# Optimization experiments

Measured on AMD Instinct MI355X. Metric: run time of the kernel, lower is better.

## Reference

```python
import jax, jax.numpy as jnp
import numpy as np

N_NODES = 100000


def _l2norm(v, eps=1e-12):
    return v / (jnp.linalg.norm(v) + eps)


def setup_inputs() -> dict:
    key = jax.random.key(0)
    k1, k2, k3, k4 = jax.random.split(key, 4)
    x = jax.random.normal(k1, (N_NODES, 128), dtype=jnp.float32)
    edge_index = jax.random.randint(k2, (2, 600000), 0, N_NODES, dtype=jnp.int64)
    # GCNConv weight [in, out] (xavier-ish scale), bias zeros (default init)
    W = jax.random.normal(k3, (128, 64), dtype=jnp.float32) * (1.0 / np.sqrt(128))
    bias = jnp.zeros((64,), dtype=jnp.float32)
    # learnable edge_wt initialized to ones (torch.ones_like(edge_weight))
    ew = jnp.ones((600000,), dtype=jnp.float32)
    # spectral-norm persistent power-iteration vector u (len = W.shape[0])
    u = jax.random.normal(k4, (128,), dtype=jnp.float32)
    return {"x": x, "edge_index": edge_index, "W": W, "bias": bias, "ew": ew, "u": u}


def gcn_forward(x, edge_index, W, bias, ew, u):
    N = x.shape[0]
    # --- spectral norm: one power-iteration step (u, v under stop_gradient) ---
    v = jax.lax.stop_gradient(_l2norm(W.T @ u))          # [out]
    u2 = jax.lax.stop_gradient(_l2norm(W @ v))           # [in]
    sigma = u2 @ (W @ v)
    W_sn = W / sigma
    # --- GCNConv with sigmoid edge weights, self-loops (weight 1), sym norm ---
    w = jax.nn.sigmoid(ew)                               # [E]
    row, col = edge_index[0], edge_index[1]
    deg = jax.ops.segment_sum(w, col, num_segments=N) + 1.0  # +1 from self-loop
    dis = jax.lax.rsqrt(deg)                             # deg > 0 always
    xp = x @ W_sn                                        # [N, out]
    norm_e = dis[row] * w * dis[col]                     # [E]
    msg = xp[row] * norm_e[:, None]                      # gather + scale
    agg = jax.ops.segment_sum(msg, col, num_segments=N)  # scatter-add
    out = agg + xp * (1.0 / deg)[:, None] + bias         # self-loop norm = deg^-1
    return out


def reference(x, edge_index, W, bias, ew, u):
    return gcn_forward(x, edge_index, W, bias, ew, u)
```

## Files before the change

kernel.cpp:

```cpp
#include <hip/hip_runtime.h>
#include <math.h>


#define IN_DIM 128
#define OUT_DIM 64

#define FIXSHIFT 4294967296.0
#define CNTSHIFT 40
#define DEGMASK  ((1ull << CNTSHIFT) - 1)

typedef __attribute__((ext_vector_type(4))) short s16x4;
typedef __attribute__((ext_vector_type(8))) short s16x8;
typedef __attribute__((ext_vector_type(4))) float f32x4;

__device__ __forceinline__ short f2bf(float f) {
    unsigned int v = __float_as_uint(f);
    v = v + 0x7FFFu + ((v >> 16) & 1u);
    return (short)(v >> 16);
}
__device__ __forceinline__ float bfLo(unsigned int v) {
    return __uint_as_float(v << 16);
}
__device__ __forceinline__ float bfHi(unsigned int v) {
    return __uint_as_float(v & 0xFFFF0000u);
}

#define APITCH 136

__global__ __launch_bounds__(256) void edge_prep(const int* __restrict__ ei,
                                                 const float* __restrict__ ew,
                                                 unsigned long long* __restrict__ packed,
                                                 int* __restrict__ slot,
                                                 int E) {
    const int e = blockIdx.x * 256 + threadIdx.x;
    if (e >= E) return;
    const float w = 1.f / (1.f + expf(-ew[e]));
    const int col = ei[E + e];
    const unsigned long long inc =
        (1ull << CNTSHIFT) | (unsigned long long)((double)w * FIXSHIFT);
    const unsigned long long old = atomicAdd(&packed[col], inc);
    slot[e] = (int)(old >> CNTSHIFT);
}

__global__ __launch_bounds__(256) void gemm_fused(const float* __restrict__ x,
                                                  const float* __restrict__ W,
                                                  const float* __restrict__ u,
                                                  const unsigned long long* __restrict__ packed,
                                                  unsigned short* __restrict__ xps,
                                                  int* __restrict__ pos,
                                                  int* __restrict__ btot,
                                                  float* __restrict__ inv_sigma,
                                                  int N, int NB) {
    __shared__ __align__(16) short As[64 * APITCH];
    __shared__ __align__(16) short Wt[64 * APITCH];

    const int t = threadIdx.x;
    const int bid = blockIdx.x;
    const int ntile = (N + 63) >> 6;

    if (bid < ntile) {
        const int r0 = bid * 64;
        {
            const int rl = t >> 2;
            const int qk = t & 3;
            const int grow = min(r0 + rl, N - 1);
            const float4* src = (const float4*)(x + (size_t)grow * IN_DIM + qk * 32);
            short* dst = &As[rl * APITCH + qk * 32];
            #pragma unroll
            for (int i = 0; i < 8; ++i) {
                const float4 v = src[i];
                s16x4 s4;
                s4.x = f2bf(v.x); s4.y = f2bf(v.y);
                s4.z = f2bf(v.z); s4.w = f2bf(v.w);
                *(s16x4*)(dst + i * 4) = s4;
            }
        }
        {
            #pragma unroll
            for (int p = 0; p < 2; ++p) {
                const int k  = p * 64 + (t >> 2);
                const int n0 = (t & 3) * 16;
                const float4* wsrc = (const float4*)(W + (size_t)k * OUT_DIM + n0);
                #pragma unroll
                for (int i = 0; i < 4; ++i) {
                    const float4 v = wsrc[i];
                    Wt[(n0 + 4 * i + 0) * APITCH + k] = f2bf(v.x);
                    Wt[(n0 + 4 * i + 1) * APITCH + k] = f2bf(v.y);
                    Wt[(n0 + 4 * i + 2) * APITCH + k] = f2bf(v.z);
                    Wt[(n0 + 4 * i + 3) * APITCH + k] = f2bf(v.w);
                }
            }
        }
        __syncthreads();

        const int wave = t >> 6;
        const int lane = t & 63;
        const int m    = lane & 15;
        const int quad = lane >> 4;

        f32x4 acc[4];
        #pragma unroll
        for (int ct = 0; ct < 4; ++ct) acc[ct] = (f32x4){0.f, 0.f, 0.f, 0.f};

        const short* Abase = &As[(wave * 16 + m) * APITCH + quad * 8];
        const short* Bbase = &Wt[m * APITCH + quad * 8];

        #pragma unroll
        for (int kc = 0; kc < 4; ++kc) {
            const s16x8 a = *(const s16x8*)(Abase + kc * 32);
            #pragma unroll
            for (int ct = 0; ct < 4; ++ct) {
                const s16x8 b = *(const s16x8*)(Bbase + ct * 16 * APITCH + kc * 32);
                acc[ct] = __builtin_amdgcn_mfma_f32_16x16x32_bf16(a, b, acc[ct], 0, 0, 0);
            }
        }

        #pragma unroll
        for (int r = 0; r < 4; ++r) {
            const int grow = r0 + wave * 16 + quad * 4 + r;
            const int gc = min(grow, N - 1);
            const unsigned long long p = packed[gc];
            const float deg = (float)((double)(p & DEGMASK) * (1.0 / FIXSHIFT));
            const float dis = rsqrtf(deg + 1.f);
            if (grow < N) {
                #pragma unroll
                for (int ct = 0; ct < 4; ++ct)
                    xps[(size_t)grow * OUT_DIM + ct * 16 + m] =
                        (unsigned short)f2bf(acc[ct][r] * dis);
            }
        }
    }

    if (bid < NB) {
        __syncthreads();
        int* s = (int*)As;
        const int i0 = bid * 1024 + t * 4;
        int v[4]; int sum = 0;
        #pragma unroll
        for (int j = 0; j < 4; ++j) {
            unsigned long long pk = (i0 + j < N) ? packed[i0 + j] : 0ull;
            v[j] = (int)(pk >> CNTSHIFT);
            sum += v[j];
        }
        s[t] = sum;
        __syncthreads();
        for (int off = 1; off < 256; off <<= 1) {
            int add = (t >= off) ? s[t - off] : 0;
            __syncthreads();
            s[t] += add;
            __syncthreads();
        }
        int excl = s[t] - sum;
        #pragma unroll
        for (int j = 0; j < 4; ++j) {
            if (i0 + j < N) pos[i0 + j] = excl;
            excl += v[j];
        }
        if (t == 255) btot[bid] = s[255];
    } else if (bid == NB) {
        __syncthreads();
        float* red = (float*)As;
        float* vsh = (float*)Wt;
        {
            const int j = t & 63;
            const int i0 = (t >> 6) * 32;
            float tv = 0.f;
            #pragma unroll 8
            for (int i = 0; i < 32; ++i) tv += W[(i0 + i) * OUT_DIM + j] * u[i0 + i];
            red[t] = tv;
        }
        __syncthreads();
        float tvj = 0.f;
        if (t < 64) tvj = red[t] + red[t + 64] + red[t + 128] + red[t + 192];
        __syncthreads();
        red[t] = (t < 64) ? tvj * tvj : 0.f;
        __syncthreads();
        for (int sr = 128; sr > 0; sr >>= 1) {
            if (t < sr) red[t] += red[t + sr];
            __syncthreads();
        }
        const float nv = sqrtf(red[0]) + 1e-12f;
        __syncthreads();
        if (t < 64) vsh[t] = tvj / nv;
        __syncthreads();
        float wv = 0.f;
        if (t < 128) {
            #pragma unroll 8
            for (int j = 0; j < OUT_DIM; ++j) wv += W[t * OUT_DIM + j] * vsh[j];
        }
        red[t] = (t < 128) ? wv * wv : 0.f;
        __syncthreads();
        for (int sr = 128; sr > 0; sr >>= 1) {
            if (t < sr) red[t] += red[t + sr];
            __syncthreads();
        }
        if (t == 0) {
            const float s2 = red[0];
            const float sn = sqrtf(s2);
            inv_sigma[0] = (sn + 1e-12f) / s2;
        }
    }
}

__global__ __launch_bounds__(256) void permute(const int* __restrict__ ei,
                                               const float* __restrict__ ew,
                                               const int* __restrict__ pos,
                                               const int* __restrict__ btot,
                                               const int* __restrict__ slot,
                                               int2* __restrict__ spk,
                                               int E, int NB) {
    __shared__ int sb[128];
    __shared__ int bex[128];
    const int t = threadIdx.x;

    int own = 0;
    if (t < 128) {
        own = (t < NB) ? btot[t] : 0;
        sb[t] = own;
    }
    __syncthreads();
    for (int off = 1; off < 128; off <<= 1) {
        int add = 0;
        if (t < 128 && t >= off) add = sb[t - off];
        __syncthreads();
        if (t < 128) sb[t] += add;
        __syncthreads();
    }
    if (t < 128) bex[t] = sb[t] - own;
    __syncthreads();

    const int e = blockIdx.x * 256 + t;
    if (e >= E) return;
    const int row = ei[e];
    const int col = ei[E + e];
    const float w = 1.f / (1.f + expf(-ew[e]));
    const int p = pos[col] + bex[col >> 10] + slot[e];
    int2 pk; pk.x = row; pk.y = __float_as_int(w);
    spk[p] = pk;
}

__global__ __launch_bounds__(256) void gather(const int2* __restrict__ spk,
                                              const int* __restrict__ pos,
                                              const int* __restrict__ btot,
                                              const unsigned long long* __restrict__ packed,
                                              const uint4* __restrict__ xps128,
                                              const float* __restrict__ bias,
                                              const float* __restrict__ inv_sigma,
                                              float* __restrict__ out,
                                              int N, int NB) {
    __shared__ int rr[128];
    const int t = threadIdx.x;
    const int q  = t >> 3;
    const int el = t & 7;
    const int n = blockIdx.x * 32 + q;

    unsigned long long p = 0ull;
    int posn = 0;
    uint4 sv = {0u, 0u, 0u, 0u};
    if (n < N) {
        p = packed[n];
        posn = pos[n];
        sv = xps128[(size_t)n * 8 + el];
    }
    const float isg = inv_sigma[0];

    const int K = (blockIdx.x * 32) >> 10;
    if (t < 128) rr[t] = (t < K) ? btot[t] : 0;
    __syncthreads();
    for (int sr = 64; sr > 0; sr >>= 1) {
        if (t < sr) rr[t] += rr[t + sr];
        __syncthreads();
    }
    const int bsum = rr[0];

    if (n >= N) return;

    const int c = (int)(p >> CNTSHIFT);
    const float deg = (float)((double)(p & DEGMASK) * (1.0 / FIXSHIFT));
    const int st = posn + bsum;

    float a0 = 0.f, a1 = 0.f, a2 = 0.f, a3 = 0.f;
    float a4 = 0.f, a5 = 0.f, a6 = 0.f, a7 = 0.f;

    for (int j0 = 0; j0 < c; j0 += 8) {
        const int rem = c - j0;
        int2 e; e.x = 0; e.y = 0;
        if (el < rem) e = spk[st + j0 + el];

        #pragma unroll
        for (int k = 0; k < 8; k += 4) {
            if (!__any(rem > k)) break;
            #pragma unroll
            for (int kk = 0; kk < 4; ++kk) {
                const int row = __shfl(e.x, k + kk, 8);
                const float w = __int_as_float(__shfl(e.y, k + kk, 8));
                const uint4 a = xps128[(size_t)row * 8 + el];
                a0 += bfLo(a.x) * w;
                a1 += bfHi(a.x) * w;
                a2 += bfLo(a.y) * w;
                a3 += bfHi(a.y) * w;
                a4 += bfLo(a.z) * w;
                a5 += bfHi(a.z) * w;
                a6 += bfLo(a.w) * w;
                a7 += bfHi(a.w) * w;
            }
        }
    }

    const float sc = isg * rsqrtf(deg + 1.f);
    const float4 bv0 = ((const float4*)bias)[el * 2];
    const float4 bv1 = ((const float4*)bias)[el * 2 + 1];
    float4 o0, o1;
    o0.x = sc * (a0 + bfLo(sv.x)) + bv0.x;
    o0.y = sc * (a1 + bfHi(sv.x)) + bv0.y;
    o0.z = sc * (a2 + bfLo(sv.y)) + bv0.z;
    o0.w = sc * (a3 + bfHi(sv.y)) + bv0.w;
    o1.x = sc * (a4 + bfLo(sv.z)) + bv1.x;
    o1.y = sc * (a5 + bfHi(sv.z)) + bv1.y;
    o1.z = sc * (a6 + bfLo(sv.w)) + bv1.z;
    o1.w = sc * (a7 + bfHi(sv.w)) + bv1.w;
    ((float4*)out)[(size_t)n * 16 + el * 2] = o0;
    ((float4*)out)[(size_t)n * 16 + el * 2 + 1] = o1;
}

extern "C" void kernel_launch(void* const* d_in, const int* in_sizes, int n_in,
                              void* d_out, int out_size, void* d_ws, size_t ws_size,
                              hipStream_t stream) {
    const float* x    = (const float*)d_in[0];
    const int*   ei   = (const int*)d_in[1];
    const float* W    = (const float*)d_in[2];
    const float* bias = (const float*)d_in[3];
    const float* ew   = (const float*)d_in[4];
    const float* u    = (const float*)d_in[5];
    float* out = (float*)d_out;

    const int N = in_sizes[0] / IN_DIM;
    const int E = in_sizes[4];
    const int NB = (N + 1023) / 1024;
    const int EB = (E + 255) / 256;

    char* ws = (char*)d_ws;
    size_t off = 0;
    unsigned long long* packed = (unsigned long long*)(ws + off); off += (size_t)N * 8;
    int*   slot = (int*)  (ws + off); off += (size_t)E * 4;
    int*   pos  = (int*)  (ws + off); off += (size_t)N * 4;
    int*   btot = (int*)  (ws + off); off += 4096;
    float* isg  = (float*)(ws + off); off += 1024;
    int2*  spk  = (int2*) (ws + off); off += (size_t)E * 8;
    unsigned short* xps = (unsigned short*)(ws + off); off += (size_t)N * OUT_DIM * 2;

    const int ntile = (N + 63) / 64;
    const int g2 = (ntile > NB + 1) ? ntile : NB + 1;

    hipMemsetAsync(packed, 0, (size_t)N * 8, stream);
    edge_prep<<<EB, 256, 0, stream>>>(ei, ew, packed, slot, E);
    gemm_fused<<<g2, 256, 0, stream>>>(x, W, u, packed, xps, pos, btot, isg, N, NB);
    permute<<<EB, 256, 0, stream>>>(ei, ew, pos, btot, slot, spk, E, NB);
    gather<<<(N + 31) / 32, 256, 0, stream>>>(spk, pos, btot, packed,
                                              (const uint4*)xps, bias, isg, out, N, NB);
}
```

Before: 173.1 us.

## Co-schedule edge degree atomics with GEMM tiles and move source normalization to permute

Merges the edge-prep atomic pass and the x@W GEMM into one interleaved grid, so the degree counting and the GEMM run at the same time instead of one after the other. For this to work, the GEMM output is no longer scaled by the source degree. That factor is now applied per edge in permute, which reads packed[row], and the self-loop term in gather is rescaled to match. The prefix scan moves to its own small kernel, and the GEMM now loads A straight from global memory instead of staging it in LDS. The cost is an extra launch and one more random read per edge in permute.

```diff
diff --git a/kernel.cpp b/kernel.cpp
--- a/kernel.cpp
+++ b/kernel.cpp
@@ -27,140 +27,24 @@
 
 #define APITCH 136
 
-__global__ __launch_bounds__(256) void edge_prep(const int* __restrict__ ei,
-                                                 const float* __restrict__ ew,
-                                                 unsigned long long* __restrict__ packed,
-                                                 int* __restrict__ slot,
-                                                 int E) {
-    const int e = blockIdx.x * 256 + threadIdx.x;
-    if (e >= E) return;
-    const float w = 1.f / (1.f + expf(-ew[e]));
-    const int col = ei[E + e];
-    const unsigned long long inc =
-        (1ull << CNTSHIFT) | (unsigned long long)((double)w * FIXSHIFT);
-    const unsigned long long old = atomicAdd(&packed[col], inc);
-    slot[e] = (int)(old >> CNTSHIFT);
-}
-
-__global__ __launch_bounds__(256) void gemm_fused(const float* __restrict__ x,
-                                                  const float* __restrict__ W,
-                                                  const float* __restrict__ u,
-                                                  const unsigned long long* __restrict__ packed,
-                                                  unsigned short* __restrict__ xps,
-                                                  int* __restrict__ pos,
-                                                  int* __restrict__ btot,
-                                                  float* __restrict__ inv_sigma,
-                                                  int N, int NB) {
-    __shared__ __align__(16) short As[64 * APITCH];
+__global__ __launch_bounds__(256) void fused(const float* __restrict__ x,
+                                             const int* __restrict__ ei,
+                                             const float* __restrict__ W,
+                                             const float* __restrict__ ew,
+                                             const float* __restrict__ u,
+                                             unsigned long long* __restrict__ packed,
+                                             int* __restrict__ slot,
+                                             unsigned short* __restrict__ xps,
+                                             float* __restrict__ inv_sigma,
+                                             int N, int E, int ntile, int G) {
     __shared__ __align__(16) short Wt[64 * APITCH];
 
     const int t = threadIdx.x;
     const int bid = blockIdx.x;
-    const int ntile = (N + 63) >> 6;
-
-    if (bid < ntile) {
-        const int r0 = bid * 64;
-        {
-            const int rl = t >> 2;
-            const int qk = t & 3;
-            const int grow = min(r0 + rl, N - 1);
-            const float4* src = (const float4*)(x + (size_t)grow * IN_DIM + qk * 32);
-            short* dst = &As[rl * APITCH + qk * 32];
-            #pragma unroll
-            for (int i = 0; i < 8; ++i) {
-                const float4 v = src[i];
-                s16x4 s4;
-                s4.x = f2bf(v.x); s4.y = f2bf(v.y);
-                s4.z = f2bf(v.z); s4.w = f2bf(v.w);
-                *(s16x4*)(dst + i * 4) = s4;
-            }
-        }
-        {
-            #pragma unroll
-            for (int p = 0; p < 2; ++p) {
-                const int k  = p * 64 + (t >> 2);
-                const int n0 = (t & 3) * 16;
-                const float4* wsrc = (const float4*)(W + (size_t)k * OUT_DIM + n0);
-                #pragma unroll
-                for (int i = 0; i < 4; ++i) {
-                    const float4 v = wsrc[i];
-                    Wt[(n0 + 4 * i + 0) * APITCH + k] = f2bf(v.x);
-                    Wt[(n0 + 4 * i + 1) * APITCH + k] = f2bf(v.y);
-                    Wt[(n0 + 4 * i + 2) * APITCH + k] = f2bf(v.z);
-                    Wt[(n0 + 4 * i + 3) * APITCH + k] = f2bf(v.w);
-                }
-            }
-        }
-        __syncthreads();
-
-        const int wave = t >> 6;
-        const int lane = t & 63;
-        const int m    = lane & 15;
-        const int quad = lane >> 4;
-
-        f32x4 acc[4];
-        #pragma unroll
-        for (int ct = 0; ct < 4; ++ct) acc[ct] = (f32x4){0.f, 0.f, 0.f, 0.f};
-
-        const short* Abase = &As[(wave * 16 + m) * APITCH + quad * 8];
-        const short* Bbase = &Wt[m * APITCH + quad * 8];
-
-        #pragma unroll
-        for (int kc = 0; kc < 4; ++kc) {
-            const s16x8 a = *(const s16x8*)(Abase + kc * 32);
-            #pragma unroll
-            for (int ct = 0; ct < 4; ++ct) {
-                const s16x8 b = *(const s16x8*)(Bbase + ct * 16 * APITCH + kc * 32);
-                acc[ct] = __builtin_amdgcn_mfma_f32_16x16x32_bf16(a, b, acc[ct], 0, 0, 0);
-            }
-        }
-
-        #pragma unroll
-        for (int r = 0; r < 4; ++r) {
-            const int grow = r0 + wave * 16 + quad * 4 + r;
-            const int gc = min(grow, N - 1);
-            const unsigned long long p = packed[gc];
-            const float deg = (float)((double)(p & DEGMASK) * (1.0 / FIXSHIFT));
-            const float dis = rsqrtf(deg + 1.f);
-            if (grow < N) {
-                #pragma unroll
-                for (int ct = 0; ct < 4; ++ct)
-                    xps[(size_t)grow * OUT_DIM + ct * 16 + m] =
-                        (unsigned short)f2bf(acc[ct][r] * dis);
-            }
-        }
-    }
-
-    if (bid < NB) {
-        __syncthreads();
-        int* s = (int*)As;
-        const int i0 = bid * 1024 + t * 4;
-        int v[4]; int sum = 0;
-        #pragma unroll
-        for (int j = 0; j < 4; ++j) {
-            unsigned long long pk = (i0 + j < N) ? packed[i0 + j] : 0ull;
-            v[j] = (int)(pk >> CNTSHIFT);
-            sum += v[j];
-        }
-        s[t] = sum;
-        __syncthreads();
-        for (int off = 1; off < 256; off <<= 1) {
-            int add = (t >= off) ? s[t - off] : 0;
-            __syncthreads();
-            s[t] += add;
-            __syncthreads();
-        }
-        int excl = s[t] - sum;
-        #pragma unroll
-        for (int j = 0; j < 4; ++j) {
-            if (i0 + j < N) pos[i0 + j] = excl;
-            excl += v[j];
-        }
-        if (t == 255) btot[bid] = s[255];
-    } else if (bid == NB) {
-        __syncthreads();
-        float* red = (float*)As;
-        float* vsh = (float*)Wt;
+
+    if (bid == G - 1) {
+        float* red = (float*)Wt;
+        float* vsh = (float*)(Wt + 512);
         {
             const int j = t & 63;
             const int i0 = (t >> 6) * 32;
@@ -199,7 +83,114 @@
             const float sn = sqrtf(s2);
             inv_sigma[0] = (sn + 1e-12f) / s2;
         }
-    }
+        return;
+    }
+
+    const int pair = bid >> 1;
+
+    if ((bid & 1) == 0) {
+        const int e = pair * 256 + t;
+        if (e >= E) return;
+        const float w = 1.f / (1.f + expf(-ew[e]));
+        const int col = ei[E + e];
+        const unsigned long long inc =
+            (1ull << CNTSHIFT) | (unsigned long long)((double)w * FIXSHIFT);
+        const unsigned long long old = atomicAdd(&packed[col], inc);
+        slot[e] = (int)(old >> CNTSHIFT);
+        return;
+    }
+
+    const int tile = pair;
+    if (tile >= ntile) return;
+    const int r0 = tile * 64;
+
+    {
+        #pragma unroll
+        for (int p = 0; p < 2; ++p) {
+            const int k  = p * 64 + (t >> 2);
+            const int n0 = (t & 3) * 16;
+            const float4* wsrc = (const float4*)(W + (size_t)k * OUT_DIM + n0);
+            #pragma unroll
+            for (int i = 0; i < 4; ++i) {
+                const float4 v = wsrc[i];
+                Wt[(n0 + 4 * i + 0) * APITCH + k] = f2bf(v.x);
+                Wt[(n0 + 4 * i + 1) * APITCH + k] = f2bf(v.y);
+                Wt[(n0 + 4 * i + 2) * APITCH + k] = f2bf(v.z);
+                Wt[(n0 + 4 * i + 3) * APITCH + k] = f2bf(v.w);
+            }
+        }
+    }
+    __syncthreads();
+
+    const int wave = t >> 6;
+    const int lane = t & 63;
+    const int m    = lane & 15;
+    const int quad = lane >> 4;
+
+    const int grow_a = min(r0 + wave * 16 + m, N - 1);
+    const float* arow = x + (size_t)grow_a * IN_DIM + quad * 8;
+
+    f32x4 acc[4];
+    #pragma unroll
+    for (int ct = 0; ct < 4; ++ct) acc[ct] = (f32x4){0.f, 0.f, 0.f, 0.f};
+
+    const short* Bbase = &Wt[m * APITCH + quad * 8];
+
+    #pragma unroll
+    for (int kc = 0; kc < 4; ++kc) {
+        const float4 f0 = *(const float4*)(arow + kc * 32);
+        const float4 f1 = *(const float4*)(arow + kc * 32 + 4);
+        s16x8 a;
+        a[0] = f2bf(f0.x); a[1] = f2bf(f0.y); a[2] = f2bf(f0.z); a[3] = f2bf(f0.w);
+        a[4] = f2bf(f1.x); a[5] = f2bf(f1.y); a[6] = f2bf(f1.z); a[7] = f2bf(f1.w);
+        #pragma unroll
+        for (int ct = 0; ct < 4; ++ct) {
+            const s16x8 b = *(const s16x8*)(Bbase + ct * 16 * APITCH + kc * 32);
+            acc[ct] = __builtin_amdgcn_mfma_f32_16x16x32_bf16(a, b, acc[ct], 0, 0, 0);
+        }
+    }
+
+    #pragma unroll
+    for (int r = 0; r < 4; ++r) {
+        const int grow = r0 + wave * 16 + quad * 4 + r;
+        if (grow < N) {
+            #pragma unroll
+            for (int ct = 0; ct < 4; ++ct)
+                xps[(size_t)grow * OUT_DIM + ct * 16 + m] =
+                    (unsigned short)f2bf(acc[ct][r]);
+        }
+    }
+}
+
+__global__ __launch_bounds__(256) void scan_a(const unsigned long long* __restrict__ packed,
+                                              int* __restrict__ pos,
+                                              int* __restrict__ btot,
+                                              int N) {
+    __shared__ int s[256];
+    const int t = threadIdx.x;
+    const int i0 = blockIdx.x * 1024 + t * 4;
+    int v[4]; int sum = 0;
+    #pragma unroll
+    for (int j = 0; j < 4; ++j) {
+        unsigned long long p = (i0 + j < N) ? packed[i0 + j] : 0ull;
+        v[j] = (int)(p >> CNTSHIFT);
+        sum += v[j];
+    }
+    s[t] = sum;
+    __syncthreads();
+    for (int off = 1; off < 256; off <<= 1) {
+        int add = (t >= off) ? s[t - off] : 0;
+        __syncthreads();
+        s[t] += add;
+        __syncthreads();
+    }
+    int excl = s[t] - sum;
+    #pragma unroll
+    for (int j = 0; j < 4; ++j) {
+        if (i0 + j < N) pos[i0 + j] = excl;
+        excl += v[j];
+    }
+    if (t == 255) btot[blockIdx.x] = s[255];
 }
 
 __global__ __launch_bounds__(256) void permute(const int* __restrict__ ei,
@@ -207,6 +198,7 @@
                                                const int* __restrict__ pos,
                                                const int* __restrict__ btot,
                                                const int* __restrict__ slot,
+                                               const unsigned long long* __restrict__ packed,
                                                int2* __restrict__ spk,
                                                int E, int NB) {
     __shared__ int sb[128];
@@ -234,8 +226,11 @@
     const int row = ei[e];
     const int col = ei[E + e];
     const float w = 1.f / (1.f + expf(-ew[e]));
+    const unsigned long long pr = packed[row];
+    const float degr = (float)((double)(pr & DEGMASK) * (1.0 / FIXSHIFT));
+    const float wfull = w * rsqrtf(degr + 1.f);
     const int p = pos[col] + bex[col >> 10] + slot[e];
-    int2 pk; pk.x = row; pk.y = __float_as_int(w);
+    int2 pk; pk.x = row; pk.y = __float_as_int(wfull);
     spk[p] = pk;
 }
 
@@ -307,18 +302,20 @@
         }
     }
 
-    const float sc = isg * rsqrtf(deg + 1.f);
+    const float dfull = deg + 1.f;
+    const float dis_n = rsqrtf(dfull);
+    const float invd  = 1.f / dfull;
     const float4 bv0 = ((const float4*)bias)[el * 2];
     const float4 bv1 = ((const float4*)bias)[el * 2 + 1];
     float4 o0, o1;
-    o0.x = sc * (a0 + bfLo(sv.x)) + bv0.x;
-    o0.y = sc * (a1 + bfHi(sv.x)) + bv0.y;
-    o0.z = sc * (a2 + bfLo(sv.y)) + bv0.z;
-    o0.w = sc * (a3 + bfHi(sv.y)) + bv0.w;
-    o1.x = sc * (a4 + bfLo(sv.z)) + bv1.x;
-    o1.y = sc * (a5 + bfHi(sv.z)) + bv1.y;
-    o1.z = sc * (a6 + bfLo(sv.w)) + bv1.z;
-    o1.w = sc * (a7 + bfHi(sv.w)) + bv1.w;
+    o0.x = isg * (dis_n * a0 + bfLo(sv.x) * invd) + bv0.x;
+    o0.y = isg * (dis_n * a1 + bfHi(sv.x) * invd) + bv0.y;
+    o0.z = isg * (dis_n * a2 + bfLo(sv.y) * invd) + bv0.z;
+    o0.w = isg * (dis_n * a3 + bfHi(sv.y) * invd) + bv0.w;
+    o1.x = isg * (dis_n * a4 + bfLo(sv.z) * invd) + bv1.x;
+    o1.y = isg * (dis_n * a5 + bfHi(sv.z) * invd) + bv1.y;
+    o1.z = isg * (dis_n * a6 + bfLo(sv.w) * invd) + bv1.z;
+    o1.w = isg * (dis_n * a7 + bfHi(sv.w) * invd) + bv1.w;
     ((float4*)out)[(size_t)n * 16 + el * 2] = o0;
     ((float4*)out)[(size_t)n * 16 + el * 2 + 1] = o1;
 }
@@ -338,6 +335,7 @@
     const int E = in_sizes[4];
     const int NB = (N + 1023) / 1024;
     const int EB = (E + 255) / 256;
+    const int ntile = (N + 63) / 64;
 
     char* ws = (char*)d_ws;
     size_t off = 0;
@@ -349,13 +347,14 @@
     int2*  spk  = (int2*) (ws + off); off += (size_t)E * 8;
     unsigned short* xps = (unsigned short*)(ws + off); off += (size_t)N * OUT_DIM * 2;
 
-    const int ntile = (N + 63) / 64;
-    const int g2 = (ntile > NB + 1) ? ntile : NB + 1;
+    const int mx = (EB > ntile) ? EB : ntile;
+    const int G = 2 * mx + 1;
 
     hipMemsetAsync(packed, 0, (size_t)N * 8, stream);
-    edge_prep<<<EB, 256, 0, stream>>>(ei, ew, packed, slot, E);
-    gemm_fused<<<g2, 256, 0, stream>>>(x, W, u, packed, xps, pos, btot, isg, N, NB);
-    permute<<<EB, 256, 0, stream>>>(ei, ew, pos, btot, slot, spk, E, NB);
+    fused<<<G, 256, 0, stream>>>(x, ei, W, ew, u, packed, slot, xps, isg,
+                                 N, E, ntile, G);
+    scan_a<<<NB, 256, 0, stream>>>(packed, pos, btot, N);
+    permute<<<EB, 256, 0, stream>>>(ei, ew, pos, btot, slot, packed, spk, E, NB);
     gather<<<(N + 31) / 32, 256, 0, stream>>>(spk, pos, btot, packed,
                                               (const uint4*)xps, bias, isg, out, N, NB);
 }
```

After: 163.9 us. -5.3%, faster.
